# Kernel optimization log

Measured on AMD Instinct MI355X. Metric: run time of the kernel, lower is better.

Reference implementation:

```python
import jax, jax.numpy as jnp
import numpy as np

B, N, D = 8, 1024, 1024
H, HD = 16, 64          # n_heads, head_dim = D // H
FF = 2 * D              # SwiGLU hidden dim (ffn_dim_mult=2)
EPS = 1e-5


def setup_inputs() -> dict:
    key = jax.random.key(0)
    ks = jax.random.split(key, 10)
    s = 0.02
    return {
        "x": jax.random.normal(ks[0], (B, N, D), dtype=jnp.float32),
        "attn_norm_scale": jnp.ones((D,), jnp.float32),
        "ffn_norm_scale": jnp.ones((D,), jnp.float32),
        "wq": jax.random.normal(ks[1], (D, D), jnp.float32) * s,
        "bq": jnp.zeros((D,), jnp.float32),
        "wk": jax.random.normal(ks[2], (D, D), jnp.float32) * s,
        "bk": jnp.zeros((D,), jnp.float32),
        "wv": jax.random.normal(ks[3], (D, D), jnp.float32) * s,
        "bv": jnp.zeros((D,), jnp.float32),
        "wo": jax.random.normal(ks[4], (D, D), jnp.float32) * s,
        "bo": jnp.zeros((D,), jnp.float32),
        "w_uv": jax.random.normal(ks[5], (D, 2 * FF), jnp.float32) * s,
        "w_out": jax.random.normal(ks[6], (FF, D), jnp.float32) * s,
    }


def _rmsnorm(x, scale):
    xf = x.astype(jnp.float32)
    y = xf * jax.lax.rsqrt(jnp.mean(xf * xf, axis=-1, keepdims=True) + EPS)
    return scale * y.astype(x.dtype)


def reference(x, attn_norm_scale, ffn_norm_scale, wq, bq, wk, bk, wv, bv,
              wo, bo, w_uv, w_out):
    # FFT2D: fft over channel dim then token dim, keep real part
    x = jnp.fft.fft(jnp.fft.fft(x, axis=-1), axis=-2).real.astype(jnp.float32)

    # --- self attention with pre-RMSNorm and residual ---
    xn = _rmsnorm(x, attn_norm_scale)
    q = (xn @ wq + bq).reshape(B, N, H, HD)
    k = (xn @ wk + bk).reshape(B, N, H, HD)
    v = (xn @ wv + bv).reshape(B, N, H, HD)
    scores = jnp.einsum('bnhd,bmhd->bhnm', q, k) / np.sqrt(HD).astype(np.float32)
    attn = jax.nn.softmax(scores, axis=-1)
    o = jnp.einsum('bhnm,bmhd->bnhd', attn, v).reshape(B, N, D)
    x = (o @ wo + bo) + x

    # --- SwiGLU FFN with pre-RMSNorm and residual ---
    xn = _rmsnorm(x, ffn_norm_scale)
    uv = xn @ w_uv                      # [B, N, 2*FF]
    u, vg = uv[..., :FF], uv[..., FF:]
    x = (jax.nn.silu(u) * vg) @ w_out + x
    return x
```

## Files before the change

kernel.cpp:

```cpp
#include <hip/hip_runtime.h>
#include <stdint.h>

typedef unsigned short u16;
typedef __attribute__((ext_vector_type(8))) __bf16 bf16x8;
typedef __attribute__((ext_vector_type(4))) float f32x4;
typedef __attribute__((ext_vector_type(8))) u16 u16x8;

static __device__ __forceinline__ u16 f2bf(float f){
  uint32_t x = __builtin_bit_cast(uint32_t, f);
  x = (x + 0x7FFFu + ((x >> 16) & 1u)) >> 16;
  return (u16)x;
}
static __device__ __forceinline__ u16 f2bf_fast(float f){
  uint32_t x = __builtin_bit_cast(uint32_t, f);
  return (u16)((x + 0x8000u) >> 16);
}
static __device__ __forceinline__ float bf2f(u16 h){
  uint32_t x = ((uint32_t)h) << 16;
  return __builtin_bit_cast(float, x);
}
static __device__ __forceinline__ f32x4 mfma16(bf16x8 a, bf16x8 b, f32x4 c){
  return __builtin_amdgcn_mfma_f32_16x16x32_bf16(a, b, c, 0, 0, 0);
}
static __device__ __forceinline__ void gload16(const void* g, void* l){
  __builtin_amdgcn_global_load_lds(
      (const __attribute__((address_space(1))) void*)(uintptr_t)g,
      (__attribute__((address_space(3))) void*)(uint32_t)(uintptr_t)l,
      16, 0, 0);
}

__global__ void k_tables(u16* __restrict__ C, u16* __restrict__ S, u16* __restrict__ Sn){
  int n = blockIdx.x;
  int m0 = threadIdx.x * 4;
  #pragma unroll
  for (int i = 0; i < 4; ++i){
    int m = m0 + i;
    int ph = (n * m) & 1023;
    float a = (float)ph * (1.0f / 512.0f);
    float c = cospif(a), s = sinpif(a);
    int idx = n * 1024 + m;
    C[idx] = f2bf(c); S[idx] = f2bf(s); Sn[idx] = f2bf(-s);
  }
}

__global__ void k_tcvt(const float* __restrict__ in, u16* __restrict__ out,
                       int R, int Cc, int64_t inB, int64_t outB){
  __shared__ float t[32][33];
  const float* ip = in + (int64_t)blockIdx.z * inB;
  u16* op = out + (int64_t)blockIdx.z * outB;
  int tc = blockIdx.x * 32, tr = blockIdx.y * 32;
  int lx = threadIdx.x & 31, ly = threadIdx.x >> 5;
  #pragma unroll
  for (int i = 0; i < 32; i += 8)
    t[ly + i][lx] = ip[(int64_t)(tr + ly + i) * Cc + tc + lx];
  __syncthreads();
  #pragma unroll
  for (int i = 0; i < 32; i += 8)
    op[(int64_t)(tc + ly + i) * R + tr + lx] = f2bf(t[lx][ly + i]);
}

__global__ void k_tcvtW(const float* __restrict__ in, u16* __restrict__ out){
  __shared__ float t[32][33];
  int tc = blockIdx.x * 32, tr = blockIdx.y * 32;
  int lx = threadIdx.x & 31, ly = threadIdx.x >> 5;
  #pragma unroll
  for (int i = 0; i < 32; i += 8)
    t[ly + i][lx] = in[(int64_t)(tr + ly + i) * 4096 + tc + lx];
  __syncthreads();
  #pragma unroll
  for (int i = 0; i < 32; i += 8){
    int c = tc + ly + i;
    int pr = (c < 2048) ? ((c >> 4) * 32 + (c & 15))
                        : (((c - 2048) >> 4) * 32 + 16 + ((c - 2048) & 15));
    out[(int64_t)pr * 1024 + tr + lx] = f2bf(t[lx][ly + i]);
  }
}

__global__ void k_bias3(const float* __restrict__ a, const float* __restrict__ b,
                        const float* __restrict__ c, float* __restrict__ o){
  int i = blockIdx.x * 256 + threadIdx.x;
  o[i] = i < 1024 ? a[i] : (i < 2048 ? b[i - 1024] : c[i - 2048]);
}

__global__ __launch_bounds__(256) void k_rmsnorm(const float* __restrict__ x,
                                                 const float* __restrict__ sc,
                                                 u16* __restrict__ out){
  int r = blockIdx.x;
  const float4* px = (const float4*)(x + (int64_t)r * 1024);
  float4 v = px[threadIdx.x];
  float ss = v.x*v.x + v.y*v.y + v.z*v.z + v.w*v.w;
  #pragma unroll
  for (int o = 1; o < 64; o <<= 1) ss += __shfl_xor(ss, o);
  __shared__ float red[4];
  if ((threadIdx.x & 63) == 0) red[threadIdx.x >> 6] = ss;
  __syncthreads();
  float tot = red[0] + red[1] + red[2] + red[3];
  float rs = rsqrtf(tot * (1.0f / 1024.0f) + 1e-5f);
  float4 s4 = ((const float4*)sc)[threadIdx.x];
  ushort4 ov;
  ov.x = f2bf(v.x * rs * s4.x); ov.y = f2bf(v.y * rs * s4.y);
  ov.z = f2bf(v.z * rs * s4.z); ov.w = f2bf(v.w * rs * s4.w);
  ((ushort4*)(out + (int64_t)r * 1024))[threadIdx.x] = ov;
}

template<int BM, bool SILU>
__global__ __launch_bounds__(512, 2) void k_gemm3(
    const u16* __restrict__ A0, const u16* __restrict__ A1,
    const u16* __restrict__ B0, const u16* __restrict__ B1,
    void* Cout, const float* __restrict__ bias, const float* resid,
    int nkt, int ktSplit, int lda, int ldb, int ldc,
    int64_t aB, int64_t bB, int64_t cB, int outBf16)
{
  constexpr int MR = BM / 32;
  constexpr int ABUF = BM * 128;
  constexpr int BBUF = 32768;
  __shared__ char smem[2 * ABUF + 2 * BBUF];
  char* Abase = smem;
  char* Bbase = smem + 2 * ABUF;

  int z = blockIdx.z;
  int nwg = gridDim.x * gridDim.y;
  int bid = blockIdx.y * gridDim.x + blockIdx.x;
  int sw = (bid & 7) * (nwg >> 3) + (bid >> 3);
  int bx = sw % gridDim.x, by = sw / gridDim.x;

  int64_t aOff = (int64_t)z * aB, bOff = (int64_t)z * bB, cOff = (int64_t)z * cB;
  int tm = by * BM, tn = bx * 256;
  int tid = threadIdx.x;
  int lane = tid & 63, w = tid >> 6;
  int lr = lane & 15, lg = lane >> 4;
  int wOffM = (w >> 2) * (MR * 16);
  int wOffN = (w & 3) * 64;

  int sline = tid >> 3;
  int skg8 = (((tid & 7) ^ (sline & 7)) * 8);

  int aRB = (wOffM + lr) * 128 + ((lg ^ (lr & 7)) * 16);
  int bRB = (wOffN + lr) * 128 + ((lg ^ (lr & 7)) * 16);

  auto stA = [&](int st, int h){
    const u16* Ap; int k0;
    if (st < ktSplit){ Ap = A0 + aOff; k0 = st * 64; }
    else             { Ap = A1 + aOff; k0 = (st - ktSplit) * 64; }
    const u16* s = Ap + (int64_t)(tm + h * 128) * lda + k0;
    char* d = Abase + (st & 1) * ABUF + h * 16384 + tid * 16;
    gload16(s + (int64_t)sline * lda + skg8, d);
    gload16(s + (int64_t)(sline + 64) * lda + skg8, d + 8192);
  };
  auto stB = [&](int st, int h){
    const u16* Bp; int k0;
    if (st < ktSplit){ Bp = B0 + bOff; k0 = st * 64; }
    else             { Bp = B1 + bOff; k0 = (st - ktSplit) * 64; }
    const u16* s = Bp + (int64_t)(tn + h * 128) * ldb + k0;
    char* d = Bbase + (st & 1) * BBUF + h * 16384 + tid * 16;
    gload16(s + (int64_t)sline * ldb + skg8, d);
    gload16(s + (int64_t)(sline + 64) * ldb + skg8, d + 8192);
  };

  const f32x4 fz = {0.f, 0.f, 0.f, 0.f};
  f32x4 acc[MR][4];
  #pragma unroll
  for (int i = 0; i < MR; ++i)
    #pragma unroll
    for (int j = 0; j < 4; ++j) acc[i][j] = fz;

  stA(0, 0); if constexpr (BM == 256) stA(0, 1);
  stB(0, 0); stB(0, 1);
  stA(1, 0); if constexpr (BM == 256) stA(1, 1);
  stB(1, 0); stB(1, 1);
  if constexpr (BM == 256) asm volatile("s_waitcnt vmcnt(8)" ::: "memory");
  else                     asm volatile("s_waitcnt vmcnt(6)" ::: "memory");
  __builtin_amdgcn_s_barrier();

  for (int kt = 0; kt < nkt; ++kt){
    const char* Ab = Abase + (kt & 1) * ABUF;
    const char* Bb = Bbase + (kt & 1) * BBUF;
    int st = kt + 2;
    bool doSt = st < nkt;
    bf16x8 bl[2][2], bh[2][2];

    if constexpr (BM == 256){
      bf16x8 al[4][2], ah[4][2];
      #pragma unroll
      for (int i = 0; i < 4; ++i)
        #pragma unroll
        for (int kc = 0; kc < 2; ++kc)
          al[i][kc] = *(const bf16x8*)(Ab + ((aRB + i * 2048) ^ (kc << 6)));
      #pragma unroll
      for (int j = 0; j < 2; ++j)
        #pragma unroll
        for (int kc = 0; kc < 2; ++kc)
          bl[j][kc] = *(const bf16x8*)(Bb + ((bRB + j * 2048) ^ (kc << 6)));
      __builtin_amdgcn_s_barrier();
      __builtin_amdgcn_s_setprio(1);
      #pragma unroll
      for (int i = 0; i < 4; ++i)
        #pragma unroll
        for (int j = 0; j < 2; ++j)
          #pragma unroll
          for (int kc = 0; kc < 2; ++kc)
            acc[i][j] = mfma16(al[i][kc], bl[j][kc], acc[i][j]);
      __builtin_amdgcn_s_setprio(0);
      __builtin_amdgcn_s_barrier();
      #pragma unroll
      for (int j = 0; j < 2; ++j)
        #pragma unroll
        for (int kc = 0; kc < 2; ++kc)
          bh[j][kc] = *(const bf16x8*)(Bb + ((bRB + (j + 2) * 2048) ^ (kc << 6)));
      if (doSt){ stA(st, 0); stB(st, 0); }
      __builtin_amdgcn_s_barrier();
      __builtin_amdgcn_s_setprio(1);
      #pragma unroll
      for (int i = 0; i < 4; ++i)
        #pragma unroll
        for (int j = 0; j < 2; ++j)
          #pragma unroll
          for (int kc = 0; kc < 2; ++kc)
            acc[i][j + 2] = mfma16(al[i][kc], bh[j][kc], acc[i][j + 2]);
      __builtin_amdgcn_s_setprio(0);
      __builtin_amdgcn_s_barrier();
      #pragma unroll
      for (int i = 0; i < 4; ++i)
        #pragma unroll
        for (int kc = 0; kc < 2; ++kc)
          ah[i][kc] = *(const bf16x8*)(Ab + ((aRB + (i + 4) * 2048) ^ (kc << 6)));
      if (doSt) stB(st, 1);
      __builtin_amdgcn_s_barrier();
      __builtin_amdgcn_s_setprio(1);
      #pragma unroll
      for (int i = 0; i < 4; ++i)
        #pragma unroll
        for (int j = 0; j < 2; ++j)
          #pragma unroll
          for (int kc = 0; kc < 2; ++kc)
            acc[i + 4][j] = mfma16(ah[i][kc], bl[j][kc], acc[i + 4][j]);
      __builtin_amdgcn_s_setprio(0);
      __builtin_amdgcn_s_barrier();
      if (doSt) stA(st, 1);
      __builtin_amdgcn_s_barrier();
      __builtin_amdgcn_s_setprio(1);
      #pragma unroll
      for (int i = 0; i < 4; ++i)
        #pragma unroll
        for (int j = 0; j < 2; ++j)
          #pragma unroll
          for (int kc = 0; kc < 2; ++kc)
            acc[i + 4][j + 2] = mfma16(ah[i][kc], bh[j][kc], acc[i + 4][j + 2]);
      __builtin_amdgcn_s_setprio(0);
      if (doSt) asm volatile("s_waitcnt vmcnt(8)" ::: "memory");
      else      asm volatile("s_waitcnt vmcnt(0)" ::: "memory");
      __builtin_amdgcn_s_barrier();
    } else {
      bf16x8 al[4][2];
      #pragma unroll
      for (int i = 0; i < 4; ++i)
        #pragma unroll
        for (int kc = 0; kc < 2; ++kc)
          al[i][kc] = *(const bf16x8*)(Ab + ((aRB + i * 2048) ^ (kc << 6)));
      #pragma unroll
      for (int j = 0; j < 2; ++j)
        #pragma unroll
        for (int kc = 0; kc < 2; ++kc)
          bl[j][kc] = *(const bf16x8*)(Bb + ((bRB + j * 2048) ^ (kc << 6)));
      __builtin_amdgcn_s_barrier();
      __builtin_amdgcn_s_setprio(1);
      #pragma unroll
      for (int i = 0; i < 4; ++i)
        #pragma unroll
        for (int j = 0; j < 2; ++j)
          #pragma unroll
          for (int kc = 0; kc < 2; ++kc)
            acc[i][j] = mfma16(al[i][kc], bl[j][kc], acc[i][j]);
      __builtin_amdgcn_s_setprio(0);
      __builtin_amdgcn_s_barrier();
      #pragma unroll
      for (int j = 0; j < 2; ++j)
        #pragma unroll
        for (int kc = 0; kc < 2; ++kc)
          bh[j][kc] = *(const bf16x8*)(Bb + ((bRB + (j + 2) * 2048) ^ (kc << 6)));
      if (doSt){ stA(st, 0); stB(st, 0); stB(st, 1); }
      __builtin_amdgcn_s_barrier();
      __builtin_amdgcn_s_setprio(1);
      #pragma unroll
      for (int i = 0; i < 4; ++i)
        #pragma unroll
        for (int j = 0; j < 2; ++j)
          #pragma unroll
          for (int kc = 0; kc < 2; ++kc)
            acc[i][j + 2] = mfma16(al[i][kc], bh[j][kc], acc[i][j + 2]);
      __builtin_amdgcn_s_setprio(0);
      if (doSt) asm volatile("s_waitcnt vmcnt(6)" ::: "memory");
      else      asm volatile("s_waitcnt vmcnt(0)" ::: "memory");
      __builtin_amdgcn_s_barrier();
    }
  }

  if constexpr (SILU){
    #pragma unroll
    for (int i = 0; i < MR; ++i){
      int colBase = ((tn + wOffN) >> 1) + lr;
      #pragma unroll
      for (int jj = 0; jj < 4; ++jj){
        int row = tm + wOffM + i * 16 + lg * 4 + jj;
        #pragma unroll
        for (int jp = 0; jp < 2; ++jp){
          float u = acc[i][jp * 2][jj], v = acc[i][jp * 2 + 1][jj];
          float s = u / (1.0f + __expf(-u));
          ((u16*)Cout)[(int64_t)row * ldc + colBase + jp * 16] = f2bf(s * v);
        }
      }
    }
  } else {
    #pragma unroll
    for (int i = 0; i < MR; ++i){
      #pragma unroll
      for (int j = 0; j < 4; ++j){
        int col = tn + wOffN + j * 16 + lr;
        float badd = bias ? bias[col] : 0.0f;
        #pragma unroll
        for (int jj = 0; jj < 4; ++jj){
          int row = tm + wOffM + i * 16 + lg * 4 + jj;
          int64_t idx = cOff + (int64_t)row * ldc + col;
          float v = acc[i][j][jj] + badd;
          if (resid) v += resid[idx];
          if (outBf16) ((u16*)Cout)[idx] = f2bf(v);
          else         ((float*)Cout)[idx] = v;
        }
      }
    }
  }
}

__global__ __launch_bounds__(256) void k_vtrans(const u16* __restrict__ qkv,
                                                u16* __restrict__ vt){
  __shared__ u16 T[64 * 65];
  int bh = blockIdx.y; int b = bh >> 4, h = bh & 15;
  int kt = blockIdx.x;
  int t = threadIdx.x;
  const u16* src = qkv + (int64_t)(b * 1024 + kt * 64) * 3072 + 2048 + h * 64;
  #pragma unroll
  for (int i = 0; i < 16; ++i){
    int idx = i * 256 + t;
    int r = idx >> 6, c = idx & 63;
    T[r * 65 + c] = src[(int64_t)r * 3072 + c];
  }
  __syncthreads();
  u16* dst = vt + (int64_t)bh * 65536 + kt * 64;
  #pragma unroll
  for (int i = 0; i < 16; ++i){
    int idx = i * 256 + t;
    int dr = idx >> 6, kc = idx & 63;
    dst[(int64_t)dr * 1024 + kc] = T[kc * 65 + dr];
  }
}

__global__ __launch_bounds__(256, 3) void k_attn2(const u16* __restrict__ qkv,
                                                  const u16* __restrict__ vt,
                                                  u16* __restrict__ O){
  __shared__ u16 Ks[2][4096];
  __shared__ u16 Vts[2][4096];
  __shared__ u16 Pl[4][2304];
  int bh = blockIdx.y; int b = bh >> 4, h = bh & 15;
  int qt = blockIdx.x;
  int t = threadIdx.x, w = t >> 6, lane = t & 63, lr = lane & 15, lg = lane >> 4;
  int sr = t >> 3, sl = t & 7;
  int swz = (sl ^ (sr & 7)) * 8;

  const u16* kg = qkv + (int64_t)b * 1024 * 3072 + 1024 + h * 64;
  const u16* vg = vt + (int64_t)bh * 65536;

  const u16* qrow = qkv + (int64_t)(b * 1024 + qt * 128 + w * 32 + lr) * 3072 + h * 64;
  bf16x8 aq[2][2];
  #pragma unroll
  for (int m = 0; m < 2; ++m)
    #pragma unroll
    for (int kc = 0; kc < 2; ++kc)
      aq[m][kc] = *(const bf16x8*)(qrow + (int64_t)m * 16 * 3072 + kc * 32 + lg * 8);

  const f32x4 fz = {0.f, 0.f, 0.f, 0.f};
  f32x4 o_[2][4];
  float lj[2][4];
  #pragma unroll
  for (int m = 0; m < 2; ++m){
    #pragma unroll
    for (int d = 0; d < 4; ++d) o_[m][d] = fz;
    #pragma unroll
    for (int j = 0; j < 4; ++j) lj[m][j] = 0.f;
  }

  #define STAGE(ktile, bn) do {                                                   \
    int r0 = sr, r1 = 32 + sr;                                                    \
    gload16(kg + (int64_t)((ktile) * 64 + r0) * 3072 + swz,                       \
            (char*)Ks + (bn) * 8192 + (t >> 6) * 1024);                           \
    gload16(kg + (int64_t)((ktile) * 64 + r1) * 3072 + swz,                       \
            (char*)Ks + (bn) * 8192 + 4096 + (t >> 6) * 1024);                    \
    gload16(vg + (int64_t)r0 * 1024 + (ktile) * 64 + swz,                         \
            (char*)Vts + (bn) * 8192 + (t >> 6) * 1024);                          \
    gload16(vg + (int64_t)r1 * 1024 + (ktile) * 64 + swz,                         \
            (char*)Vts + (bn) * 8192 + 4096 + (t >> 6) * 1024);                   \
  } while (0)

  STAGE(0, 0);
  __syncthreads();
  int buf = 0;
  int lsw = lr & 7;

  const float CSC = 0.1803368801111204f;
  const float MSH = 8.656170245333781f;

  #pragma unroll 1
  for (int kt = 0; kt < 16; ++kt){
    if (kt < 15) STAGE(kt + 1, buf ^ 1);

    f32x4 s[2][4];
    #pragma unroll
    for (int m = 0; m < 2; ++m)
      #pragma unroll
      for (int n = 0; n < 4; ++n) s[m][n] = fz;
    #pragma unroll
    for (int n = 0; n < 4; ++n){
      #pragma unroll
      for (int kc = 0; kc < 2; ++kc){
        bf16x8 kb = *(const bf16x8*)&Ks[buf][(n * 16 + lr) * 64 + (((kc * 4 + lg) ^ lsw) * 8)];
        s[0][n] = mfma16(aq[0][kc], kb, s[0][n]);
        s[1][n] = mfma16(aq[1][kc], kb, s[1][n]);
      }
    }

    #pragma unroll
    for (int m = 0; m < 2; ++m){
      #pragma unroll
      for (int j = 0; j < 4; ++j){
        float p0 = exp2f(fmaf(s[m][0][j], CSC, -MSH));
        float p1 = exp2f(fmaf(s[m][1][j], CSC, -MSH));
        float p2 = exp2f(fmaf(s[m][2][j], CSC, -MSH));
        float p3 = exp2f(fmaf(s[m][3][j], CSC, -MSH));
        lj[m][j] += (p0 + p1) + (p2 + p3);
        u16* pb = &Pl[w][(m * 16 + lg * 4 + j) * 72 + lr];
        pb[0]  = f2bf_fast(p0); pb[16] = f2bf_fast(p1);
        pb[32] = f2bf_fast(p2); pb[48] = f2bf_fast(p3);
      }
    }
    asm volatile("s_waitcnt lgkmcnt(0)" ::: "memory");
    __builtin_amdgcn_sched_barrier(0);

    #pragma unroll
    for (int kc = 0; kc < 2; ++kc){
      bf16x8 pa0 = *(const bf16x8*)&Pl[w][(lr) * 72 + kc * 32 + lg * 8];
      bf16x8 pa1 = *(const bf16x8*)&Pl[w][(16 + lr) * 72 + kc * 32 + lg * 8];
      #pragma unroll
      for (int dt = 0; dt < 4; ++dt){
        bf16x8 vb = *(const bf16x8*)&Vts[buf][(dt * 16 + lr) * 64 + (((kc * 4 + lg) ^ lsw) * 8)];
        o_[0][dt] = mfma16(pa0, vb, o_[0][dt]);
        o_[1][dt] = mfma16(pa1, vb, o_[1][dt]);
      }
    }
    __syncthreads();
    buf ^= 1;
  }
  #undef STAGE

  u16* obase = O + (int64_t)(b * 1024 + qt * 128 + w * 32) * 1024 + h * 64;
  #pragma unroll
  for (int m = 0; m < 2; ++m){
    #pragma unroll
    for (int j = 0; j < 4; ++j){
      float l = lj[m][j];
      l += __shfl_xor(l, 1); l += __shfl_xor(l, 2);
      l += __shfl_xor(l, 4); l += __shfl_xor(l, 8);
      float inv = 1.0f / l;
      int q = m * 16 + lg * 4 + j;
      #pragma unroll
      for (int dt = 0; dt < 4; ++dt)
        obase[(int64_t)q * 1024 + dt * 16 + lr] = f2bf(o_[m][dt][j] * inv);
    }
  }
}

extern "C" void kernel_launch(void* const* d_in, const int* in_sizes, int n_in,
                              void* d_out, int out_size, void* d_ws, size_t ws_size,
                              hipStream_t stream)
{
  (void)in_sizes; (void)n_in; (void)out_size; (void)ws_size;
  const float* x    = (const float*)d_in[0];
  const float* ans  = (const float*)d_in[1];
  const float* fns  = (const float*)d_in[2];
  const float* wq   = (const float*)d_in[3];
  const float* bq   = (const float*)d_in[4];
  const float* wk   = (const float*)d_in[5];
  const float* bk   = (const float*)d_in[6];
  const float* wv   = (const float*)d_in[7];
  const float* bvv  = (const float*)d_in[8];
  const float* wo   = (const float*)d_in[9];
  const float* bo   = (const float*)d_in[10];
  const float* wuv  = (const float*)d_in[11];
  const float* wout = (const float*)d_in[12];

  char* ws = (char*)d_ws;
  const size_t MB = 1u << 20;
  const int64_t M1 = 1024 * 1024;
  u16*  xbt   = (u16*)(ws + 0 * MB);
  u16*  Xc    = (u16*)(ws + 16 * MB);
  u16*  Xs    = (u16*)(ws + 32 * MB);
  u16*  qkv   = (u16*)(ws + 0 * MB);
  u16*  g     = (u16*)(ws + 0 * MB);
  u16*  xn2   = (u16*)(ws + 32 * MB);
  float* Y    = (float*)(ws + 48 * MB);
  u16*  xn    = (u16*)(ws + 80 * MB);
  u16*  vtg   = (u16*)(ws + 80 * MB);
  u16*  Obuf  = (u16*)(ws + 96 * MB);
  u16*  Cb    = (u16*)(ws + 112 * MB);
  u16*  Sb    = (u16*)(ws + 114 * MB);
  u16*  Snb   = (u16*)(ws + 116 * MB);
  u16*  wqkvt = (u16*)(ws + 118 * MB);
  u16*  wot   = (u16*)(ws + 124 * MB);
  u16*  wuvt  = (u16*)(ws + 126 * MB);
  u16*  woutt = (u16*)(ws + 134 * MB);
  float* bqkv = (float*)(ws + 138 * MB);
  float* outF = (float*)d_out;

  k_tables<<<dim3(1024), 256, 0, stream>>>(Cb, Sb, Snb);
  k_tcvt<<<dim3(32, 32, 8), 256, 0, stream>>>(x, xbt, 1024, 1024, M1, M1);
  k_tcvt<<<dim3(32, 32, 1), 256, 0, stream>>>(wq, wqkvt,          1024, 1024, 0, 0);
  k_tcvt<<<dim3(32, 32, 1), 256, 0, stream>>>(wk, wqkvt + M1,     1024, 1024, 0, 0);
  k_tcvt<<<dim3(32, 32, 1), 256, 0, stream>>>(wv, wqkvt + 2 * M1, 1024, 1024, 0, 0);
  k_tcvt<<<dim3(32, 32, 1), 256, 0, stream>>>(wo, wot, 1024, 1024, 0, 0);
  k_tcvtW<<<dim3(128, 32), 256, 0, stream>>>(wuv, wuvt);
  k_tcvt<<<dim3(32, 64, 1), 256, 0, stream>>>(wout, woutt, 2048, 1024, 0, 0);
  k_bias3<<<dim3(12), 256, 0, stream>>>(bq, bk, bvv, bqkv);

  k_gemm3<128,false><<<dim3(4, 8, 8), 512, 0, stream>>>(Cb, Cb, xbt, xbt, Xc, nullptr, nullptr,
      16, 16, 1024, 1024, 1024, 0, M1, M1, 1);
  k_gemm3<128,false><<<dim3(4, 8, 8), 512, 0, stream>>>(Sb, Sb, xbt, xbt, Xs, nullptr, nullptr,
      16, 16, 1024, 1024, 1024, 0, M1, M1, 1);
  k_gemm3<128,false><<<dim3(4, 64, 1), 512, 0, stream>>>(Xc, Xs, Cb, Snb, Y, nullptr, nullptr,
      32, 16, 1024, 1024, 1024, 0, 0, 0, 0);

  k_rmsnorm<<<dim3(8192), 256, 0, stream>>>(Y, ans, xn);
  k_gemm3<128,false><<<dim3(12, 64, 1), 512, 0, stream>>>(xn, xn, wqkvt, wqkvt, qkv, bqkv, nullptr,
      16, 16, 1024, 1024, 3072, 0, 0, 0, 1);
  k_vtrans<<<dim3(16, 128), 256, 0, stream>>>(qkv, vtg);
  k_attn2<<<dim3(8, 128), 256, 0, stream>>>(qkv, vtg, Obuf);
  k_gemm3<128,false><<<dim3(4, 64, 1), 512, 0, stream>>>(Obuf, Obuf, wot, wot, d_out, bo, Y,
      16, 16, 1024, 1024, 1024, 0, 0, 0, 0);

  k_rmsnorm<<<dim3(8192), 256, 0, stream>>>(outF, fns, xn2);
  k_gemm3<256,true><<<dim3(16, 32, 1), 512, 0, stream>>>(xn2, xn2, wuvt, wuvt, g, nullptr, nullptr,
      16, 16, 1024, 1024, 2048, 0, 0, 0, 1);
  k_gemm3<128,false><<<dim3(4, 64, 1), 512, 0, stream>>>(g, g, woutt, woutt, d_out, nullptr, outF,
      32, 32, 2048, 2048, 1024, 0, 0, 0, 0);
}
```

Measured before the change: 460.4 us.

## Exploit real-input DFT symmetry to halve token-axis FFT GEMM work

The 2D real-part DFT is restructured so only the rows k <= 512 (640 rows with padding) of the cosine and sine products are computed, fused into one batched GEMM with a row split between tables. A second GEMM builds the partial sums, and a new finishing kernel reconstructs all 1024 rows by conjugate symmetry (k and 1024-k share terms with a sign flip), writing the float residual and the fused RMSNorm output in the same pass. This removes the separate rmsnorm launch, the negated-sine table and roughly half the FFT GEMM FLOPs. The GEMM loader now chooses its operand by row tile instead of by K step and precomputes addresses, which simplifies the inner-loop address math. The cost is an extra intermediate buffer and an additional bf16 rounding of intermediates before the final sum.

```diff
diff --git a/kernel.cpp b/kernel.cpp
--- a/kernel.cpp
+++ b/kernel.cpp
@@ -29,7 +29,7 @@
       16, 0, 0);
 }
 
-__global__ void k_tables(u16* __restrict__ C, u16* __restrict__ S, u16* __restrict__ Sn){
+__global__ void k_tables(u16* __restrict__ C, u16* __restrict__ S){
   int n = blockIdx.x;
   int m0 = threadIdx.x * 4;
   #pragma unroll
@@ -37,9 +37,8 @@
     int m = m0 + i;
     int ph = (n * m) & 1023;
     float a = (float)ph * (1.0f / 512.0f);
-    float c = cospif(a), s = sinpif(a);
     int idx = n * 1024 + m;
-    C[idx] = f2bf(c); S[idx] = f2bf(s); Sn[idx] = f2bf(-s);
+    C[idx] = f2bf(cospif(a)); S[idx] = f2bf(sinpif(a));
   }
 }
 
@@ -103,12 +102,47 @@
   ((ushort4*)(out + (int64_t)r * 1024))[threadIdx.x] = ov;
 }
 
+__global__ __launch_bounds__(256) void k_fftfin(const u16* __restrict__ Uw,
+                                                const float* __restrict__ sc,
+                                                float* __restrict__ Y,
+                                                u16* __restrict__ xn){
+  int row = blockIdx.x;
+  int b = row >> 10, k = row & 1023;
+  int kp = (k <= 512) ? k : 1024 - k;
+  float sgn = (k <= 512) ? -1.0f : 1.0f;
+  const u16* ub = Uw + (int64_t)b * (1280 * 1024) + (int64_t)kp * 1024;
+  const u16* wb = ub + 640 * 1024;
+  int c4 = threadIdx.x * 4;
+  ushort4 uu = *(const ushort4*)(ub + c4);
+  ushort4 ww = *(const ushort4*)(wb + c4);
+  float y0 = bf2f(uu.x) + sgn * bf2f(ww.x);
+  float y1 = bf2f(uu.y) + sgn * bf2f(ww.y);
+  float y2 = bf2f(uu.z) + sgn * bf2f(ww.z);
+  float y3 = bf2f(uu.w) + sgn * bf2f(ww.w);
+  float ss = y0*y0 + y1*y1 + y2*y2 + y3*y3;
+  #pragma unroll
+  for (int o = 1; o < 64; o <<= 1) ss += __shfl_xor(ss, o);
+  __shared__ float red[4];
+  if ((threadIdx.x & 63) == 0) red[threadIdx.x >> 6] = ss;
+  __syncthreads();
+  float tot = red[0] + red[1] + red[2] + red[3];
+  float rs = rsqrtf(tot * (1.0f / 1024.0f) + 1e-5f);
+  float4 s4 = ((const float4*)sc)[threadIdx.x];
+  float4 yo; yo.x = y0; yo.y = y1; yo.z = y2; yo.w = y3;
+  ((float4*)(Y + (int64_t)row * 1024))[threadIdx.x] = yo;
+  ushort4 ov;
+  ov.x = f2bf(y0 * rs * s4.x); ov.y = f2bf(y1 * rs * s4.y);
+  ov.z = f2bf(y2 * rs * s4.z); ov.w = f2bf(y3 * rs * s4.w);
+  ((ushort4*)(xn + (int64_t)row * 1024))[threadIdx.x] = ov;
+}
+
+
 template<int BM, bool SILU>
 __global__ __launch_bounds__(512, 2) void k_gemm3(
     const u16* __restrict__ A0, const u16* __restrict__ A1,
     const u16* __restrict__ B0, const u16* __restrict__ B1,
     void* Cout, const float* __restrict__ bias, const float* resid,
-    int nkt, int ktSplit, int lda, int ldb, int ldc,
+    int nkt, int rowSplit, int lda, int ldb, int ldc,
     int64_t aB, int64_t bB, int64_t cB, int outBf16)
 {
   constexpr int MR = BM / 32;
@@ -124,7 +158,6 @@
   int sw = (bid & 7) * (nwg >> 3) + (bid >> 3);
   int bx = sw % gridDim.x, by = sw / gridDim.x;
 
-  int64_t aOff = (int64_t)z * aB, bOff = (int64_t)z * bB, cOff = (int64_t)z * cB;
   int tm = by * BM, tn = bx * 256;
   int tid = threadIdx.x;
   int lane = tid & 63, w = tid >> 6;
@@ -132,29 +165,29 @@
   int wOffM = (w >> 2) * (MR * 16);
   int wOffN = (w & 3) * 64;
 
+  const u16* Ap = ((tm < rowSplit) ? A0 : A1) + (int64_t)z * aB;
+  const u16* Bp = ((tm < rowSplit) ? B0 : B1) + (int64_t)z * bB;
+  int64_t cOff = (int64_t)z * cB;
+
   int sline = tid >> 3;
   int skg8 = (((tid & 7) ^ (sline & 7)) * 8);
+  int64_t aAdr = (int64_t)(tm + sline) * lda + skg8;
+  int64_t bAdr = (int64_t)(tn + sline) * ldb + skg8;
 
   int aRB = (wOffM + lr) * 128 + ((lg ^ (lr & 7)) * 16);
   int bRB = (wOffN + lr) * 128 + ((lg ^ (lr & 7)) * 16);
 
   auto stA = [&](int st, int h){
-    const u16* Ap; int k0;
-    if (st < ktSplit){ Ap = A0 + aOff; k0 = st * 64; }
-    else             { Ap = A1 + aOff; k0 = (st - ktSplit) * 64; }
-    const u16* s = Ap + (int64_t)(tm + h * 128) * lda + k0;
     char* d = Abase + (st & 1) * ABUF + h * 16384 + tid * 16;
-    gload16(s + (int64_t)sline * lda + skg8, d);
-    gload16(s + (int64_t)(sline + 64) * lda + skg8, d + 8192);
+    const u16* s = Ap + aAdr + (int64_t)(h * 128) * lda + st * 64;
+    gload16(s, d);
+    gload16(s + (int64_t)64 * lda, d + 8192);
   };
   auto stB = [&](int st, int h){
-    const u16* Bp; int k0;
-    if (st < ktSplit){ Bp = B0 + bOff; k0 = st * 64; }
-    else             { Bp = B1 + bOff; k0 = (st - ktSplit) * 64; }
-    const u16* s = Bp + (int64_t)(tn + h * 128) * ldb + k0;
     char* d = Bbase + (st & 1) * BBUF + h * 16384 + tid * 16;
-    gload16(s + (int64_t)sline * ldb + skg8, d);
-    gload16(s + (int64_t)(sline + 64) * ldb + skg8, d + 8192);
+    const u16* s = Bp + bAdr + (int64_t)(h * 128) * ldb + st * 64;
+    gload16(s, d);
+    gload16(s + (int64_t)64 * ldb, d + 8192);
   };
 
   const f32x4 fz = {0.f, 0.f, 0.f, 0.f};
@@ -499,27 +532,27 @@
   char* ws = (char*)d_ws;
   const size_t MB = 1u << 20;
   const int64_t M1 = 1024 * 1024;
+  const int64_t FB = (int64_t)1280 * 1024;
+  const int BIG = 1 << 30;
   u16*  xbt   = (u16*)(ws + 0 * MB);
-  u16*  Xc    = (u16*)(ws + 16 * MB);
-  u16*  Xs    = (u16*)(ws + 32 * MB);
+  u16*  Xcs   = (u16*)(ws + 16 * MB);
+  u16*  Uw    = (u16*)(ws + 36 * MB);
+  u16*  xn    = (u16*)(ws + 56 * MB);
   u16*  qkv   = (u16*)(ws + 0 * MB);
-  u16*  g     = (u16*)(ws + 0 * MB);
-  u16*  xn2   = (u16*)(ws + 32 * MB);
-  float* Y    = (float*)(ws + 48 * MB);
-  u16*  xn    = (u16*)(ws + 80 * MB);
-  u16*  vtg   = (u16*)(ws + 80 * MB);
-  u16*  Obuf  = (u16*)(ws + 96 * MB);
-  u16*  Cb    = (u16*)(ws + 112 * MB);
-  u16*  Sb    = (u16*)(ws + 114 * MB);
-  u16*  Snb   = (u16*)(ws + 116 * MB);
-  u16*  wqkvt = (u16*)(ws + 118 * MB);
-  u16*  wot   = (u16*)(ws + 124 * MB);
-  u16*  wuvt  = (u16*)(ws + 126 * MB);
-  u16*  woutt = (u16*)(ws + 134 * MB);
-  float* bqkv = (float*)(ws + 138 * MB);
+  u16*  vtg   = (u16*)(ws + 72 * MB);
+  u16*  Obuf  = (u16*)(ws + 88 * MB);
+  u16*  xn2   = (u16*)(ws + 0 * MB);
+  u16*  g     = (u16*)(ws + 16 * MB);
+  u16*  Cb    = (u16*)(ws + 104 * MB);
+  u16*  Sb    = (u16*)(ws + 106 * MB);
+  u16*  wqkvt = (u16*)(ws + 108 * MB);
+  u16*  wot   = (u16*)(ws + 114 * MB);
+  u16*  wuvt  = (u16*)(ws + 116 * MB);
+  u16*  woutt = (u16*)(ws + 124 * MB);
+  float* bqkv = (float*)(ws + 128 * MB);
   float* outF = (float*)d_out;
 
-  k_tables<<<dim3(1024), 256, 0, stream>>>(Cb, Sb, Snb);
+  k_tables<<<dim3(1024), 256, 0, stream>>>(Cb, Sb);
   k_tcvt<<<dim3(32, 32, 8), 256, 0, stream>>>(x, xbt, 1024, 1024, M1, M1);
   k_tcvt<<<dim3(32, 32, 1), 256, 0, stream>>>(wq, wqkvt,          1024, 1024, 0, 0);
   k_tcvt<<<dim3(32, 32, 1), 256, 0, stream>>>(wk, wqkvt + M1,     1024, 1024, 0, 0);
@@ -529,24 +562,28 @@
   k_tcvt<<<dim3(32, 64, 1), 256, 0, stream>>>(wout, woutt, 2048, 1024, 0, 0);
   k_bias3<<<dim3(12), 256, 0, stream>>>(bq, bk, bvv, bqkv);
 
-  k_gemm3<128,false><<<dim3(4, 8, 8), 512, 0, stream>>>(Cb, Cb, xbt, xbt, Xc, nullptr, nullptr,
-      16, 16, 1024, 1024, 1024, 0, M1, M1, 1);
-  k_gemm3<128,false><<<dim3(4, 8, 8), 512, 0, stream>>>(Sb, Sb, xbt, xbt, Xs, nullptr, nullptr,
-      16, 16, 1024, 1024, 1024, 0, M1, M1, 1);
-  k_gemm3<128,false><<<dim3(4, 64, 1), 512, 0, stream>>>(Xc, Xs, Cb, Snb, Y, nullptr, nullptr,
-      32, 16, 1024, 1024, 1024, 0, 0, 0, 0);
-
-  k_rmsnorm<<<dim3(8192), 256, 0, stream>>>(Y, ans, xn);
-  k_gemm3<128,false><<<dim3(12, 64, 1), 512, 0, stream>>>(xn, xn, wqkvt, wqkvt, qkv, bqkv, nullptr,
-      16, 16, 1024, 1024, 3072, 0, 0, 0, 1);
+  k_gemm3<128,false><<<dim3(4, 10, 8), 512, 0, stream>>>(
+      Cb, Sb - 640 * 1024, xbt, xbt, Xcs, nullptr, nullptr,
+      16, 640, 1024, 1024, 1024, 0, M1, FB, 1);
+  k_gemm3<128,false><<<dim3(4, 10, 8), 512, 0, stream>>>(
+      Xcs, Xcs, Cb, Sb, Uw, nullptr, nullptr,
+      16, 640, 1024, 1024, 1024, FB, 0, FB, 1);
+  k_fftfin<<<dim3(8192), 256, 0, stream>>>(Uw, ans, outF, xn);
+
+  k_gemm3<128,false><<<dim3(12, 64, 1), 512, 0, stream>>>(
+      xn, xn, wqkvt, wqkvt, qkv, bqkv, nullptr,
+      16, BIG, 1024, 1024, 3072, 0, 0, 0, 1);
   k_vtrans<<<dim3(16, 128), 256, 0, stream>>>(qkv, vtg);
   k_attn2<<<dim3(8, 128), 256, 0, stream>>>(qkv, vtg, Obuf);
-  k_gemm3<128,false><<<dim3(4, 64, 1), 512, 0, stream>>>(Obuf, Obuf, wot, wot, d_out, bo, Y,
-      16, 16, 1024, 1024, 1024, 0, 0, 0, 0);
+  k_gemm3<128,false><<<dim3(4, 64, 1), 512, 0, stream>>>(
+      Obuf, Obuf, wot, wot, d_out, bo, outF,
+      16, BIG, 1024, 1024, 1024, 0, 0, 0, 0);
 
   k_rmsnorm<<<dim3(8192), 256, 0, stream>>>(outF, fns, xn2);
-  k_gemm3<256,true><<<dim3(16, 32, 1), 512, 0, stream>>>(xn2, xn2, wuvt, wuvt, g, nullptr, nullptr,
-      16, 16, 1024, 1024, 2048, 0, 0, 0, 1);
-  k_gemm3<128,false><<<dim3(4, 64, 1), 512, 0, stream>>>(g, g, woutt, woutt, d_out, nullptr, outF,
-      32, 32, 2048, 2048, 1024, 0, 0, 0, 0);
-}
+  k_gemm3<256,true><<<dim3(16, 32, 1), 512, 0, stream>>>(
+      xn2, xn2, wuvt, wuvt, g, nullptr, nullptr,
+      16, BIG, 1024, 1024, 2048, 0, 0, 0, 1);
+  k_gemm3<128,false><<<dim3(4, 64, 1), 512, 0, stream>>>(
+      g, g, woutt, woutt, d_out, nullptr, outF,
+      32, BIG, 2048, 2048, 1024, 0, 0, 0, 0);
+}
```

Result: faster. 451.3 us (-2.0%).
